# Optimization experiments

Hardware: AMD Instinct MI355X
Metric: run time of the kernel (lower is better)

## Reference

```python
import math
import jax, jax.numpy as jnp
import numpy as np

V, D, DEPTH, H, DH, FF = 32000, 1024, 4, 16, 64, 4096
B, N = 1, 2048


def setup_inputs() -> dict:
    key = jax.random.key(0)
    ks = jax.random.split(key, 8)
    s = 0.02
    return {
        "x": jax.random.randint(ks[0], (B, N), 0, V, dtype=jnp.int32),
        "token_emb": jax.random.normal(ks[1], (V, D), jnp.float32) * s,
        "attn_gamma": jnp.ones((DEPTH, D), jnp.float32),
        "w_qkv": jax.random.normal(ks[2], (DEPTH, D, 3 * H * DH), jnp.float32) * s,
        "w_attn_out": jax.random.normal(ks[3], (DEPTH, H * DH, D), jnp.float32) * s,
        "ff_gamma": jnp.ones((DEPTH, D), jnp.float32),
        "w_ff1": jax.random.normal(ks[4], (DEPTH, D, FF), jnp.float32) * s,
        "b_ff1": jnp.zeros((DEPTH, FF), jnp.float32),
        "w_ff2": jax.random.normal(ks[5], (DEPTH, FF, D), jnp.float32) * s,
        "b_ff2": jnp.zeros((DEPTH, D), jnp.float32),
        "final_gamma": jnp.ones((D,), jnp.float32),
        "w_logits": jax.random.normal(ks[6], (D, V), jnp.float32) * s,
    }


def rms_norm(x, gamma):
    # F.normalize(x, dim=-1) * sqrt(D) * gamma
    norm = jnp.sqrt(jnp.sum(x * x, axis=-1, keepdims=True))
    return x / jnp.maximum(norm, 1e-12) * (x.shape[-1] ** 0.5) * gamma


def rope_cos_sin(n, dh, dtype):
    # lucidrains rotary-embedding-torch default: interleaved pairs
    inv_freq = 1.0 / (10000.0 ** (jnp.arange(0, dh, 2, dtype=jnp.float32) / dh))
    freqs = jnp.arange(n, dtype=jnp.float32)[:, None] * inv_freq[None, :]  # [n, dh/2]
    freqs = jnp.repeat(freqs, 2, axis=-1)  # [n, dh]
    return jnp.cos(freqs).astype(dtype), jnp.sin(freqs).astype(dtype)


def rotate_half(x):
    x1 = x[..., 0::2]
    x2 = x[..., 1::2]
    return jnp.stack((-x2, x1), axis=-1).reshape(x.shape)


def apply_rope(t, cos, sin):
    # t: [b, h, n, dh]; cos/sin: [n, dh]
    return t * cos[None, None] + rotate_half(t) * sin[None, None]


def decoder_forward(x, token_emb, attn_gamma, w_qkv, w_attn_out, ff_gamma,
                    w_ff1, b_ff1, w_ff2, b_ff2, final_gamma, w_logits):
    b, n = x.shape
    h = token_emb[x]  # [b, n, D]
    cos, sin = rope_cos_sin(n, DH, h.dtype)
    causal = jnp.triu(jnp.ones((n, n), bool), k=1)
    scale = DH ** -0.5
    neg = -jnp.finfo(h.dtype).max
    for l in range(DEPTH):
        # attention block
        xn = rms_norm(h, attn_gamma[l])
        qkv = xn @ w_qkv[l]  # [b, n, 3*H*DH]
        qkv = qkv.reshape(b, n, 3, H, DH).transpose(2, 0, 3, 1, 4)  # [3, b, H, n, DH]
        q, k, v = qkv[0], qkv[1], qkv[2]
        q = apply_rope(q, cos, sin)
        k = apply_rope(k, cos, sin)
        sim = jnp.einsum('bhid,bhjd->bhij', q, k) * scale
        sim = jnp.where(causal, neg, sim)
        attn = jax.nn.softmax(sim, axis=-1)
        out = jnp.einsum('bhij,bhjd->bhid', attn, v)
        out = out.transpose(0, 2, 1, 3).reshape(b, n, H * DH) @ w_attn_out[l]
        h = h + out
        # feedforward block
        fn = rms_norm(h, ff_gamma[l])
        ff = jax.nn.gelu(fn @ w_ff1[l] + b_ff1[l], approximate=False) @ w_ff2[l] + b_ff2[l]
        h = h + ff
    return rms_norm(h, final_gamma) @ w_logits


def reference(x, token_emb, attn_gamma, w_qkv, w_attn_out, ff_gamma,
              w_ff1, b_ff1, w_ff2, b_ff2, final_gamma, w_logits):
    return decoder_forward(x, token_emb, attn_gamma, w_qkv, w_attn_out, ff_gamma,
                           w_ff1, b_ff1, w_ff2, b_ff2, final_gamma, w_logits)
```

## Files before the change

### kernel.cpp

```cpp
#include <hip/hip_runtime.h>
#include <math.h>


#define NSEQ 2048
#define DMODEL 1024
#define NH 16
#define DHEAD 64
#define FFD 4096
#define VOC 32000
#define NLAYER 4

typedef unsigned short u16;
typedef short bf16x8 __attribute__((ext_vector_type(8)));
typedef float f32x4 __attribute__((ext_vector_type(4)));

__device__ __forceinline__ u16 f2bf(float f) {
  unsigned int u = __builtin_bit_cast(unsigned int, f);
  u += 0x7fffu + ((u >> 16) & 1u);
  return (u16)(u >> 16);
}

__device__ __forceinline__ void gload16(const void* g, void* l) {
  __builtin_amdgcn_global_load_lds((__attribute__((address_space(1))) void*)g,
                                   (__attribute__((address_space(3))) void*)l,
                                   16, 0, 0);
}

__device__ __forceinline__ f32x4 mfma16x32(bf16x8 a, bf16x8 b, f32x4 c) {
  return __builtin_amdgcn_mfma_f32_16x16x32_bf16(a, b, c, 0, 0, 0);
}

template <int N>
__device__ __forceinline__ void waitvm() {
  if constexpr (N == 0) asm volatile("s_waitcnt vmcnt(0)" ::: "memory");
  else if constexpr (N == 2) asm volatile("s_waitcnt vmcnt(2)" ::: "memory");
  else if constexpr (N == 3) asm volatile("s_waitcnt vmcnt(3)" ::: "memory");
  else if constexpr (N == 4) asm volatile("s_waitcnt vmcnt(4)" ::: "memory");
  else if constexpr (N == 6) asm volatile("s_waitcnt vmcnt(6)" ::: "memory");
  else if constexpr (N == 8) asm volatile("s_waitcnt vmcnt(8)" ::: "memory");
}


__global__ __launch_bounds__(256) void k_embed(const int* __restrict__ x,
                                               const float* __restrict__ emb,
                                               float* __restrict__ h) {
  const int n = blockIdx.x, t = threadIdx.x;
  const int tok = x[n];
  reinterpret_cast<float4*>(h + (size_t)n * DMODEL)[t] =
      reinterpret_cast<const float4*>(emb + (size_t)tok * DMODEL)[t];
}

__global__ void k_rope(float* __restrict__ ct, float* __restrict__ st) {
  const int n = blockIdx.x, p = threadIdx.x;
  const double inv = exp(-(double)(2 * p) / 64.0 * log(10000.0));
  const double a = (double)n * inv;
  ct[n * 32 + p] = (float)cos(a);
  st[n * 32 + p] = (float)sin(a);
}

__global__ __launch_bounds__(256) void k_transpose(const float* __restrict__ in0,
                                                   u16* __restrict__ out0,
                                                   int K, int Nc,
                                                   size_t ls_in, size_t ls_out) {
  const float* in = in0 + blockIdx.z * ls_in;
  u16* out = out0 + blockIdx.z * ls_out;
  __shared__ float tile[64][65];
  const int kb = blockIdx.x * 64, nb = blockIdx.y * 64;
  const int tr = threadIdx.x >> 4;
  const int tc = threadIdx.x & 15;
#pragma unroll
  for (int r = 0; r < 64; r += 16) {
    const float4 v = *reinterpret_cast<const float4*>(
        &in[(size_t)(kb + r + tr) * Nc + nb + tc * 4]);
    tile[r + tr][tc * 4 + 0] = v.x;
    tile[r + tr][tc * 4 + 1] = v.y;
    tile[r + tr][tc * 4 + 2] = v.z;
    tile[r + tr][tc * 4 + 3] = v.w;
  }
  __syncthreads();
#pragma unroll
  for (int r = 0; r < 64; r += 16) {
    const int n = r + tr;
    ushort4 o;
    o.x = f2bf(tile[tc * 4 + 0][n]);
    o.y = f2bf(tile[tc * 4 + 1][n]);
    o.z = f2bf(tile[tc * 4 + 2][n]);
    o.w = f2bf(tile[tc * 4 + 3][n]);
    *reinterpret_cast<ushort4*>(&out[(size_t)(nb + n) * K + kb + tc * 4]) = o;
  }
}

__global__ __launch_bounds__(256) void k_rmsnorm(const float* __restrict__ h,
                                                 const float* __restrict__ gamma,
                                                 u16* __restrict__ out) {
  __shared__ float red[4];
  const int n = blockIdx.x, t = threadIdx.x;
  const float4 v = reinterpret_cast<const float4*>(h + (size_t)n * DMODEL)[t];
  float ss = v.x * v.x + v.y * v.y + v.z * v.z + v.w * v.w;
#pragma unroll
  for (int off = 32; off; off >>= 1) ss += __shfl_down(ss, off);
  if ((t & 63) == 0) red[t >> 6] = ss;
  __syncthreads();
  const float tot = red[0] + red[1] + red[2] + red[3];
  const float inv = 32.0f / fmaxf(sqrtf(tot), 1e-12f);
  const float4 g = reinterpret_cast<const float4*>(gamma)[t];
  ushort4 o;
  o.x = f2bf(v.x * inv * g.x);
  o.y = f2bf(v.y * inv * g.y);
  o.z = f2bf(v.z * inv * g.z);
  o.w = f2bf(v.w * inv * g.w);
  reinterpret_cast<ushort4*>(out + (size_t)n * DMODEL)[t] = o;
}

#define EPI_STORE 0
#define EPI_ADD 1
#define EPI_GELU 2
#define EPI_BIAS_ADD 3
#define EPI_QKV 4

__device__ __forceinline__ bf16x8 ldsfragT(const char* base, int row, int lg) {
  return *reinterpret_cast<const bf16x8*>(
      base + row * 64 + (((lg ^ (row & 3) ^ ((row >> 2) & 3)) & 3) << 4));
}

template <int EPI, int BM, int BN>
__global__ __launch_bounds__(256) void k_gemmT(
    const u16* __restrict__ A, const u16* __restrict__ BT, int K, int Nc,
    int NMB, const float* __restrict__ bias, const float* __restrict__ add,
    float* __restrict__ outf, u16* __restrict__ outb,
    u16* __restrict__ Qr, u16* __restrict__ Kr, u16* __restrict__ VT,
    const float* __restrict__ ct, const float* __restrict__ st) {
  constexpr int MFR = BM / 32;
  constexpr int NFR = BN / 32;
  constexpr int ABYTES = BM * 64;
  constexpr int BBYTES = BN * 64;
  constexpr int BUFB = ABYTES + BBYTES;
  constexpr int SL = BM / 64 + BN / 64;
  __shared__ alignas(16) char sm[4 * BUFB];
  const int nt = K >> 5;
  const int nwg = gridDim.x;
  int swz = blockIdx.x;
  if ((nwg & 7) == 0) swz = (swz & 7) * (nwg >> 3) + (swz >> 3);
  const int mb = swz % NMB, nb = swz / NMB;
  const int m0 = mb * BM, n0 = nb * BN;

  const int tid = threadIdx.x, w = tid >> 6, lane = tid & 63;
  const int wr = w >> 1, wc = w & 1;
  const int lr = lane & 15, lg = lane >> 4;

  const int srow = tid >> 2;
  const int gslot = (tid & 3) ^ (srow & 3) ^ ((srow >> 2) & 3);
  const u16* ga0 = A + (size_t)(m0 + srow) * K + gslot * 8;
  const u16* ga1 = A + (size_t)(m0 + (BM == 128 ? 64 : 0) + srow) * K + gslot * 8;
  const u16* gb0 = BT + (size_t)(n0 + srow) * K + gslot * 8;
  const u16* gb1 = BT + (size_t)(n0 + (BN == 128 ? 64 : 0) + srow) * K + gslot * 8;
  const int ldOff = tid * 16;

  auto stage = [&](int b) {
    char* base = sm + b * BUFB;
    gload16(ga0, base + ldOff);
    if constexpr (BM == 128) gload16(ga1, base + 4096 + ldOff);
    gload16(gb0, base + ABYTES + ldOff);
    if constexpr (BN == 128) gload16(gb1, base + ABYTES + 4096 + ldOff);
    ga0 += 32; gb0 += 32;
    if constexpr (BM == 128) ga1 += 32;
    if constexpr (BN == 128) gb1 += 32;
  };

  stage(0);
  stage(1);
  stage(2);
  waitvm<2 * SL>();
  __builtin_amdgcn_s_barrier();

  f32x4 acc[MFR][NFR] = {};
  int cur = 0;
  for (int t = 0; t < nt; ++t) {
    const char* Ab = sm + cur * BUFB;
    const char* Bb = Ab + ABYTES;
    bf16x8 af[MFR], bf[NFR];
#pragma unroll
    for (int i = 0; i < MFR; ++i)
      af[i] = ldsfragT(Ab, wr * (BM / 2) + i * 16 + lr, lg);
#pragma unroll
    for (int i = 0; i < NFR; ++i)
      bf[i] = ldsfragT(Bb, wc * (BN / 2) + i * 16 + lr, lg);
    if (t + 3 < nt) stage((cur + 3) & 3);
    __builtin_amdgcn_s_setprio(1);
#pragma unroll
    for (int mi = 0; mi < MFR; ++mi)
#pragma unroll
      for (int nj = 0; nj < NFR; ++nj)
        acc[mi][nj] = mfma16x32(af[mi], bf[nj], acc[mi][nj]);
    __builtin_amdgcn_s_setprio(0);
    if (t + 1 < nt) {
      __builtin_amdgcn_sched_barrier(0);
      if (t + 3 < nt)      waitvm<2 * SL>();
      else if (t + 2 < nt) waitvm<SL>();
      else                 waitvm<0>();
      __builtin_amdgcn_s_barrier();
      __builtin_amdgcn_sched_barrier(0);
    }
    cur = (cur + 1) & 3;
  }

  if constexpr (EPI == EPI_QKV) {
    const int which = n0 >> 10;
    const int hh = ((n0 & 1023) >> 6) + wc;
#pragma unroll
    for (int mi = 0; mi < MFR; ++mi) {
#pragma unroll
      for (int nj = 0; nj < NFR; ++nj) {
        const int d = nj * 16 + lr;
#pragma unroll
        for (int r = 0; r < 4; ++r) {
          const int row = m0 + wr * (BM / 2) + mi * 16 + lg * 4 + r;
          const float v = acc[mi][nj][r];
          if (which == 2) {
            VT[((size_t)hh * DHEAD + d) * NSEQ + row] = f2bf(v);
          } else {
            const float part = __shfl_xor(v, 1);
            const float sgn = (d & 1) ? 1.0f : -1.0f;
            const float c = ct[row * 32 + (d >> 1)];
            const float s_ = st[row * 32 + (d >> 1)];
            const u16 o = f2bf(v * c + sgn * part * s_);
            u16* dst = (which == 0) ? Qr : Kr;
            dst[((size_t)hh * NSEQ + row) * DHEAD + d] = o;
          }
        }
      }
    }
    return;
  }
#pragma unroll
  for (int mi = 0; mi < MFR; ++mi) {
#pragma unroll
    for (int nj = 0; nj < NFR; ++nj) {
      const int col = n0 + wc * (BN / 2) + nj * 16 + lr;
#pragma unroll
      for (int r = 0; r < 4; ++r) {
        const int row = m0 + wr * (BM / 2) + mi * 16 + lg * 4 + r;
        const size_t idx = (size_t)row * Nc + col;
        float v = acc[mi][nj][r];
        if (EPI == EPI_GELU) {
          v += bias[col];
          v = 0.5f * v * (1.0f + erff(v * 0.70710678118654752f));
          outb[idx] = f2bf(v);
        } else if (EPI == EPI_ADD) {
          outf[idx] = v + add[idx];
        } else if (EPI == EPI_BIAS_ADD) {
          outf[idx] = v + bias[col] + add[idx];
        } else {
          outf[idx] = v;
        }
      }
    }
  }
}

template <int EPI>
__global__ __launch_bounds__(256, 2) void k_gemmW(
    const u16* __restrict__ A, const u16* __restrict__ BT, int K, int Nc,
    const float* __restrict__ bias, float* __restrict__ outf,
    u16* __restrict__ outb) {
  constexpr int ABYTES = 8192;
  constexpr int BUFB = ABYTES + 16384;
  __shared__ alignas(16) char sm[3 * BUFB];
  const int nt = K >> 5;
  const int NMB = 16;
  const int nwg = gridDim.x;
  int swz = blockIdx.x;
  if ((nwg & 7) == 0) swz = (swz & 7) * (nwg >> 3) + (swz >> 3);
  const int mb = swz % NMB, nb = swz / NMB;
  const int m0 = mb * 128, n0 = nb * 256;

  const int tid = threadIdx.x, w = tid >> 6, lane = tid & 63;
  const int wr = w >> 1, wc = w & 1;
  const int lr = lane & 15, lg = lane >> 4;

  const int srow = tid >> 2;
  const int gslot = (tid & 3) ^ (srow & 3) ^ ((srow >> 2) & 3);
  const u16* ga0 = A + (size_t)(m0 + srow) * K + gslot * 8;
  const u16* ga1 = A + (size_t)(m0 + 64 + srow) * K + gslot * 8;
  const u16* gb0 = BT + (size_t)(n0 + srow) * K + gslot * 8;
  const u16* gb1 = BT + (size_t)(n0 + 64 + srow) * K + gslot * 8;
  const u16* gb2 = BT + (size_t)(n0 + 128 + srow) * K + gslot * 8;
  const u16* gb3 = BT + (size_t)(n0 + 192 + srow) * K + gslot * 8;
  const int ldOff = tid * 16;

  auto stage = [&](int b) {
    char* base = sm + b * BUFB;
    gload16(ga0, base + ldOff);
    gload16(ga1, base + 4096 + ldOff);
    gload16(gb0, base + ABYTES + ldOff);
    gload16(gb1, base + ABYTES + 4096 + ldOff);
    gload16(gb2, base + ABYTES + 8192 + ldOff);
    gload16(gb3, base + ABYTES + 12288 + ldOff);
    ga0 += 32; ga1 += 32; gb0 += 32; gb1 += 32; gb2 += 32; gb3 += 32;
  };

  stage(0);
  stage(1);
  waitvm<6>();
  __builtin_amdgcn_s_barrier();

  f32x4 acc[4][8] = {};
  int cur = 0, nx2 = 2;
  for (int t = 0; t < nt; ++t) {
    const char* Ab = sm + cur * BUFB;
    const char* Bb = Ab + ABYTES;
    const bool pf = (t + 2 < nt);
    bf16x8 af[4], bf[8];
#pragma unroll
    for (int i = 0; i < 4; ++i)
      af[i] = ldsfragT(Ab, wr * 64 + i * 16 + lr, lg);
#pragma unroll
    for (int i = 0; i < 8; ++i)
      bf[i] = ldsfragT(Bb, wc * 128 + i * 16 + lr, lg);
    if (pf) stage(nx2);
    __builtin_amdgcn_s_setprio(1);
#pragma unroll
    for (int mi = 0; mi < 4; ++mi)
#pragma unroll
      for (int nj = 0; nj < 8; ++nj)
        acc[mi][nj] = mfma16x32(af[mi], bf[nj], acc[mi][nj]);
    __builtin_amdgcn_s_setprio(0);
    if (t + 1 < nt) {
      __builtin_amdgcn_sched_barrier(0);
      if (pf) waitvm<6>();
      else    waitvm<0>();
      __builtin_amdgcn_s_barrier();
      __builtin_amdgcn_sched_barrier(0);
    }
    cur = (cur == 2) ? 0 : cur + 1;
    nx2 = (nx2 == 2) ? 0 : nx2 + 1;
  }

#pragma unroll
  for (int mi = 0; mi < 4; ++mi) {
#pragma unroll
    for (int nj = 0; nj < 8; ++nj) {
      const int col = n0 + wc * 128 + nj * 16 + lr;
#pragma unroll
      for (int r = 0; r < 4; ++r) {
        const int row = m0 + wr * 64 + mi * 16 + lg * 4 + r;
        const size_t idx = (size_t)row * Nc + col;
        float v = acc[mi][nj][r];
        if (EPI == EPI_GELU) {
          v += bias[col];
          v = 0.5f * v * (1.0f + erff(v * 0.70710678118654752f));
          outb[idx] = f2bf(v);
        } else {
          outf[idx] = v;
        }
      }
    }
  }
}

__global__ __launch_bounds__(256) void k_attn(const u16* __restrict__ Qr,
                                              const u16* __restrict__ Kr,
                                              const u16* __restrict__ VT,
                                              u16* __restrict__ O) {
  __shared__ alignas(16) u16 Pl[4][16 * 32];
  const int id = blockIdx.x;
  int qb, hh;
  if (id < 256) { qb = id & 31; hh = id >> 5; }
  else          { qb = 31 - (id & 31); hh = 8 + ((id - 256) >> 5); }
  const int w = threadIdx.x >> 6, lane = threadIdx.x & 63;
  const int lr = lane & 15, lg = lane >> 4;
  const int q0 = qb * 64 + w * 16;
  const u16* Qh = Qr + (size_t)hh * NSEQ * DHEAD;
  const u16* Kh = Kr + (size_t)hh * NSEQ * DHEAD;
  const u16* Vh = VT + (size_t)hh * DHEAD * NSEQ;
  u16* Pw = Pl[w];

  const bf16x8 aq0 = *reinterpret_cast<const bf16x8*>(Qh + (q0 + lr) * DHEAD + lg * 8);
  const bf16x8 aq1 = *reinterpret_cast<const bf16x8*>(Qh + (q0 + lr) * DHEAD + 32 + lg * 8);

  f32x4 o0 = {}, o1 = {}, o2 = {}, o3 = {};
  float m[4], l[4];
#pragma unroll
  for (int r = 0; r < 4; ++r) { m[r] = -1e30f; l[r] = 0.0f; }

  const int jend = q0 + 15;

  auto loadK = [&](int j0, bf16x8* bk) {
    bk[0] = *reinterpret_cast<const bf16x8*>(Kh + (j0 + lr) * DHEAD + lg * 8);
    bk[1] = *reinterpret_cast<const bf16x8*>(Kh + (j0 + lr) * DHEAD + 32 + lg * 8);
    bk[2] = *reinterpret_cast<const bf16x8*>(Kh + (j0 + 16 + lr) * DHEAD + lg * 8);
    bk[3] = *reinterpret_cast<const bf16x8*>(Kh + (j0 + 16 + lr) * DHEAD + 32 + lg * 8);
  };
  auto loadV = [&](int j0, bf16x8* vv) {
    const u16* vb = Vh + j0 + lg * 8;
    vv[0] = *reinterpret_cast<const bf16x8*>(vb + (0 + lr) * NSEQ);
    vv[1] = *reinterpret_cast<const bf16x8*>(vb + (16 + lr) * NSEQ);
    vv[2] = *reinterpret_cast<const bf16x8*>(vb + (32 + lr) * NSEQ);
    vv[3] = *reinterpret_cast<const bf16x8*>(vb + (48 + lr) * NSEQ);
  };

  bf16x8 bk[4], vv[4], bkN[4], vvN[4];
  loadK(0, bk);
  loadV(0, vv);

  for (int j0 = 0; j0 <= jend; j0 += 32) {
    if (j0 + 32 <= jend) { loadK(j0 + 32, bkN); loadV(j0 + 32, vvN); }

    f32x4 s0 = {}, s1 = {};
    s0 = mfma16x32(aq0, bk[0], s0);
    s0 = mfma16x32(aq1, bk[1], s0);
    s1 = mfma16x32(aq0, bk[2], s1);
    s1 = mfma16x32(aq1, bk[3], s1);

    float sv0[4], sv1[4], pm[4];
#pragma unroll
    for (int r = 0; r < 4; ++r) {
      const int irow = q0 + lg * 4 + r;
      sv0[r] = (j0 + lr > irow) ? -1e30f : s0[r] * 0.125f;
      sv1[r] = (j0 + 16 + lr > irow) ? -1e30f : s1[r] * 0.125f;
      pm[r] = fmaxf(sv0[r], sv1[r]);
    }
#pragma unroll
    for (int off = 1; off < 16; off <<= 1)
#pragma unroll
      for (int r = 0; r < 4; ++r) pm[r] = fmaxf(pm[r], __shfl_xor(pm[r], off));
    float p0[4], p1[4], rs[4];
    f32x4 fv;
#pragma unroll
    for (int r = 0; r < 4; ++r) {
      const float mn = fmaxf(m[r], pm[r]);
      fv[r] = __expf(m[r] - mn);
      m[r] = mn;
      p0[r] = __expf(sv0[r] - mn);
      p1[r] = __expf(sv1[r] - mn);
      rs[r] = p0[r] + p1[r];
    }
#pragma unroll
    for (int off = 1; off < 16; off <<= 1)
#pragma unroll
      for (int r = 0; r < 4; ++r) rs[r] += __shfl_xor(rs[r], off);
#pragma unroll
    for (int r = 0; r < 4; ++r) l[r] = l[r] * fv[r] + rs[r];
    o0 *= fv; o1 *= fv; o2 *= fv; o3 *= fv;

#pragma unroll
    for (int r = 0; r < 4; ++r) {
      Pw[(lg * 4 + r) * 32 + lr] = f2bf(p0[r]);
      Pw[(lg * 4 + r) * 32 + 16 + lr] = f2bf(p1[r]);
    }
    const bf16x8 pa = *reinterpret_cast<const bf16x8*>(Pw + lr * 32 + lg * 8);
    o0 = mfma16x32(pa, vv[0], o0);
    o1 = mfma16x32(pa, vv[1], o1);
    o2 = mfma16x32(pa, vv[2], o2);
    o3 = mfma16x32(pa, vv[3], o3);

#pragma unroll
    for (int i = 0; i < 4; ++i) { bk[i] = bkN[i]; vv[i] = vvN[i]; }
  }

#pragma unroll
  for (int r = 0; r < 4; ++r) {
    const int row = q0 + lg * 4 + r;
    const float invl = 1.0f / l[r];
    u16* orow = O + (size_t)row * DMODEL + hh * DHEAD;
    orow[0 * 16 + lr] = f2bf(o0[r] * invl);
    orow[1 * 16 + lr] = f2bf(o1[r] * invl);
    orow[2 * 16 + lr] = f2bf(o2[r] * invl);
    orow[3 * 16 + lr] = f2bf(o3[r] * invl);
  }
}


extern "C" void kernel_launch(void* const* d_in, const int* in_sizes, int n_in,
                              void* d_out, int out_size, void* d_ws, size_t ws_size,
                              hipStream_t stream) {
  (void)in_sizes; (void)n_in;
  const int* x = (const int*)d_in[0];
  const float* emb = (const float*)d_in[1];
  const float* attn_gamma = (const float*)d_in[2];
  const float* w_qkv = (const float*)d_in[3];
  const float* w_attn_out = (const float*)d_in[4];
  const float* ff_gamma = (const float*)d_in[5];
  const float* w_ff1 = (const float*)d_in[6];
  const float* b_ff1 = (const float*)d_in[7];
  const float* w_ff2 = (const float*)d_in[8];
  const float* b_ff2 = (const float*)d_in[9];
  const float* final_gamma = (const float*)d_in[10];
  const float* w_logits = (const float*)d_in[11];
  float* out = (float*)d_out;

  const size_t EARLY_NEED = 176ull << 20;
  const size_t FINAL_NEED = 72ull << 20;
  char* earlyBase;
  char* finalBase;
  if (ws_size >= EARLY_NEED + FINAL_NEED) {
    earlyBase = (char*)d_ws;
    finalBase = (char*)d_ws + EARLY_NEED;
  } else if (ws_size >= FINAL_NEED && (size_t)out_size * 4 >= EARLY_NEED) {
    earlyBase = (char*)d_out;
    finalBase = (char*)d_ws;
  } else {
    return;
  }
  size_t eoff = 0, foff = 0;
  auto ealloc = [&](size_t b) { void* p = earlyBase + eoff; eoff += (b + 255) & ~(size_t)255; return p; };
  auto falloc = [&](size_t b) { void* p = finalBase + foff; foff += (b + 255) & ~(size_t)255; return p; };

  u16* wqkvT = (u16*)ealloc((size_t)NLAYER * 3072 * DMODEL * 2);
  u16* wattnT = (u16*)ealloc((size_t)NLAYER * DMODEL * DMODEL * 2);
  u16* wff1T = (u16*)ealloc((size_t)NLAYER * FFD * DMODEL * 2);
  u16* wff2T = (u16*)ealloc((size_t)NLAYER * DMODEL * FFD * 2);
  float* h = (float*)ealloc((size_t)NSEQ * DMODEL * 4);
  u16* Qr = (u16*)ealloc((size_t)NH * NSEQ * DHEAD * 2);
  u16* Kr = (u16*)ealloc((size_t)NH * NSEQ * DHEAD * 2);
  u16* VTb = (u16*)ealloc((size_t)NH * NSEQ * DHEAD * 2);
  u16* Ob = (u16*)ealloc((size_t)NSEQ * DMODEL * 2);
  u16* ff1b = (u16*)ealloc((size_t)NSEQ * FFD * 2);
  float* ct = (float*)ealloc((size_t)NSEQ * 32 * 4);
  float* st = (float*)ealloc((size_t)NSEQ * 32 * 4);
  u16* wlogT = (u16*)falloc((size_t)VOC * DMODEL * 2);
  u16* xn = (u16*)falloc((size_t)NSEQ * DMODEL * 2);

  k_rope<<<dim3(NSEQ), dim3(32), 0, stream>>>(ct, st);
  k_transpose<<<dim3(16, 48, NLAYER), 256, 0, stream>>>(
      w_qkv, wqkvT, DMODEL, 3072, (size_t)DMODEL * 3072, (size_t)3072 * DMODEL);
  k_transpose<<<dim3(16, 16, NLAYER), 256, 0, stream>>>(
      w_attn_out, wattnT, DMODEL, DMODEL, (size_t)DMODEL * DMODEL, (size_t)DMODEL * DMODEL);
  k_transpose<<<dim3(16, 64, NLAYER), 256, 0, stream>>>(
      w_ff1, wff1T, DMODEL, FFD, (size_t)DMODEL * FFD, (size_t)FFD * DMODEL);
  k_transpose<<<dim3(64, 16, NLAYER), 256, 0, stream>>>(
      w_ff2, wff2T, FFD, DMODEL, (size_t)FFD * DMODEL, (size_t)DMODEL * FFD);
  k_transpose<<<dim3(16, 500, 1), 256, 0, stream>>>(
      w_logits, wlogT, DMODEL, VOC, 0, 0);

  k_embed<<<dim3(NSEQ), 256, 0, stream>>>(x, emb, h);

  for (int lyr = 0; lyr < NLAYER; ++lyr) {
    k_rmsnorm<<<dim3(NSEQ), 256, 0, stream>>>(h, attn_gamma + (size_t)lyr * DMODEL, xn);
    k_gemmT<EPI_QKV, 64, 128><<<dim3(32 * 24), 256, 0, stream>>>(
        xn, wqkvT + (size_t)lyr * 3072 * DMODEL, DMODEL, 3072, 32,
        nullptr, nullptr, nullptr, nullptr, Qr, Kr, VTb, ct, st);
    k_attn<<<dim3(512), 256, 0, stream>>>(Qr, Kr, VTb, Ob);
    k_gemmT<EPI_ADD, 64, 64><<<dim3(32 * 16), 256, 0, stream>>>(
        Ob, wattnT + (size_t)lyr * DMODEL * DMODEL, DMODEL, DMODEL, 32,
        nullptr, h, h, nullptr, nullptr, nullptr, nullptr, nullptr, nullptr);
    k_rmsnorm<<<dim3(NSEQ), 256, 0, stream>>>(h, ff_gamma + (size_t)lyr * DMODEL, xn);
    k_gemmT<EPI_GELU, 64, 128><<<dim3(32 * 32), 256, 0, stream>>>(
        xn, wff1T + (size_t)lyr * FFD * DMODEL, DMODEL, FFD, 32,
        b_ff1 + (size_t)lyr * FFD, nullptr, nullptr, ff1b,
        nullptr, nullptr, nullptr, nullptr, nullptr);
    k_gemmT<EPI_BIAS_ADD, 64, 64><<<dim3(32 * 16), 256, 0, stream>>>(
        ff1b, wff2T + (size_t)lyr * DMODEL * FFD, FFD, DMODEL, 32,
        b_ff2 + (size_t)lyr * DMODEL, h, h, nullptr,
        nullptr, nullptr, nullptr, nullptr, nullptr);
  }

  k_rmsnorm<<<dim3(NSEQ), 256, 0, stream>>>(h, final_gamma, xn);
  k_gemmW<EPI_STORE><<<dim3(16 * 125), 256, 0, stream>>>(
      xn, wlogT, DMODEL, VOC, nullptr, out, nullptr);
}
```

Before: 1.205 ms.

## Split-K the FF2 GEMM with atomic residual accumulation; nontemporal weight/logit stores

The FF2 GEMM (K=4096) is split into two K halves, launched as twice as many workgroups, and each half atomically adds its partial result plus bias (first half only) into the residual h, so the separate read of the add buffer goes away. The goal is better CU occupancy for a long-K GEMM that had only 512 tiles. Separately, the weight-transpose and logits output stores become nontemporal to reduce cache pollution. Atomics add contention and make the float summation order nondeterministic.

```diff
diff --git a/kernel.cpp b/kernel.cpp
--- a/kernel.cpp
+++ b/kernel.cpp
@@ -86,7 +86,10 @@
     o.y = f2bf(tile[tc * 4 + 1][n]);
     o.z = f2bf(tile[tc * 4 + 2][n]);
     o.w = f2bf(tile[tc * 4 + 3][n]);
-    *reinterpret_cast<ushort4*>(&out[(size_t)(nb + n) * K + kb + tc * 4]) = o;
+    const unsigned long long ull = __builtin_bit_cast(unsigned long long, o);
+    __builtin_nontemporal_store(
+        ull, reinterpret_cast<unsigned long long*>(
+                 &out[(size_t)(nb + n) * K + kb + tc * 4]));
   }
 }
 
@@ -117,13 +120,14 @@
 #define EPI_GELU 2
 #define EPI_BIAS_ADD 3
 #define EPI_QKV 4
+#define EPI_ATOM 5
 
 __device__ __forceinline__ bf16x8 ldsfragT(const char* base, int row, int lg) {
   return *reinterpret_cast<const bf16x8*>(
       base + row * 64 + (((lg ^ (row & 3) ^ ((row >> 2) & 3)) & 3) << 4));
 }
 
-template <int EPI, int BM, int BN>
+template <int EPI, int BM, int BN, int KSPLIT>
 __global__ __launch_bounds__(256) void k_gemmT(
     const u16* __restrict__ A, const u16* __restrict__ BT, int K, int Nc,
     int NMB, const float* __restrict__ bias, const float* __restrict__ add,
@@ -138,11 +142,20 @@
   constexpr int SL = BM / 64 + BN / 64;
   __shared__ alignas(16) char sm[4 * BUFB];
   const int nt = K >> 5;
-  const int nwg = gridDim.x;
-  int swz = blockIdx.x;
-  if ((nwg & 7) == 0) swz = (swz & 7) * (nwg >> 3) + (swz >> 3);
+  int bid = blockIdx.x;
+  int ksp = 0;
+  int inner = gridDim.x;
+  if constexpr (KSPLIT == 2) {
+    inner = gridDim.x >> 1;
+    ksp = bid / inner;
+    bid = bid % inner;
+  }
+  int swz = bid;
+  if ((inner & 7) == 0) swz = (swz & 7) * (inner >> 3) + (swz >> 3);
   const int mb = swz % NMB, nb = swz / NMB;
   const int m0 = mb * BM, n0 = nb * BN;
+  const int lda = K * KSPLIT;
+  const size_t kofs = (size_t)ksp * K;
 
   const int tid = threadIdx.x, w = tid >> 6, lane = tid & 63;
   const int wr = w >> 1, wc = w & 1;
@@ -150,10 +163,10 @@
 
   const int srow = tid >> 2;
   const int gslot = (tid & 3) ^ (srow & 3) ^ ((srow >> 2) & 3);
-  const u16* ga0 = A + (size_t)(m0 + srow) * K + gslot * 8;
-  const u16* ga1 = A + (size_t)(m0 + (BM == 128 ? 64 : 0) + srow) * K + gslot * 8;
-  const u16* gb0 = BT + (size_t)(n0 + srow) * K + gslot * 8;
-  const u16* gb1 = BT + (size_t)(n0 + (BN == 128 ? 64 : 0) + srow) * K + gslot * 8;
+  const u16* ga0 = A + (size_t)(m0 + srow) * lda + kofs + gslot * 8;
+  const u16* ga1 = A + (size_t)(m0 + (BM == 128 ? 64 : 0) + srow) * lda + kofs + gslot * 8;
+  const u16* gb0 = BT + (size_t)(n0 + srow) * lda + kofs + gslot * 8;
+  const u16* gb1 = BT + (size_t)(n0 + (BN == 128 ? 64 : 0) + srow) * lda + kofs + gslot * 8;
   const int ldOff = tid * 16;
 
   auto stage = [&](int b) {
@@ -242,7 +255,10 @@
         const int row = m0 + wr * (BM / 2) + mi * 16 + lg * 4 + r;
         const size_t idx = (size_t)row * Nc + col;
         float v = acc[mi][nj][r];
-        if (EPI == EPI_GELU) {
+        if (EPI == EPI_ATOM) {
+          if (ksp == 0) v += bias[col];
+          atomicAdd(&outf[idx], v);
+        } else if (EPI == EPI_GELU) {
           v += bias[col];
           v = 0.5f * v * (1.0f + erff(v * 0.70710678118654752f));
           outb[idx] = f2bf(v);
@@ -351,7 +367,7 @@
           v = 0.5f * v * (1.0f + erff(v * 0.70710678118654752f));
           outb[idx] = f2bf(v);
         } else {
-          outf[idx] = v;
+          __builtin_nontemporal_store(v, &outf[idx]);
         }
       }
     }
@@ -537,21 +553,21 @@
 
   for (int lyr = 0; lyr < NLAYER; ++lyr) {
     k_rmsnorm<<<dim3(NSEQ), 256, 0, stream>>>(h, attn_gamma + (size_t)lyr * DMODEL, xn);
-    k_gemmT<EPI_QKV, 64, 128><<<dim3(32 * 24), 256, 0, stream>>>(
+    k_gemmT<EPI_QKV, 64, 128, 1><<<dim3(32 * 24), 256, 0, stream>>>(
         xn, wqkvT + (size_t)lyr * 3072 * DMODEL, DMODEL, 3072, 32,
         nullptr, nullptr, nullptr, nullptr, Qr, Kr, VTb, ct, st);
     k_attn<<<dim3(512), 256, 0, stream>>>(Qr, Kr, VTb, Ob);
-    k_gemmT<EPI_ADD, 64, 64><<<dim3(32 * 16), 256, 0, stream>>>(
+    k_gemmT<EPI_ADD, 64, 64, 1><<<dim3(32 * 16), 256, 0, stream>>>(
         Ob, wattnT + (size_t)lyr * DMODEL * DMODEL, DMODEL, DMODEL, 32,
         nullptr, h, h, nullptr, nullptr, nullptr, nullptr, nullptr, nullptr);
     k_rmsnorm<<<dim3(NSEQ), 256, 0, stream>>>(h, ff_gamma + (size_t)lyr * DMODEL, xn);
-    k_gemmT<EPI_GELU, 64, 128><<<dim3(32 * 32), 256, 0, stream>>>(
+    k_gemmT<EPI_GELU, 64, 128, 1><<<dim3(32 * 32), 256, 0, stream>>>(
         xn, wff1T + (size_t)lyr * FFD * DMODEL, DMODEL, FFD, 32,
         b_ff1 + (size_t)lyr * FFD, nullptr, nullptr, ff1b,
         nullptr, nullptr, nullptr, nullptr, nullptr);
-    k_gemmT<EPI_BIAS_ADD, 64, 64><<<dim3(32 * 16), 256, 0, stream>>>(
-        ff1b, wff2T + (size_t)lyr * DMODEL * FFD, FFD, DMODEL, 32,
-        b_ff2 + (size_t)lyr * DMODEL, h, h, nullptr,
+    k_gemmT<EPI_ATOM, 64, 64, 2><<<dim3(32 * 16 * 2), 256, 0, stream>>>(
+        ff1b, wff2T + (size_t)lyr * DMODEL * FFD, FFD / 2, DMODEL, 32,
+        b_ff2 + (size_t)lyr * DMODEL, nullptr, h, nullptr,
         nullptr, nullptr, nullptr, nullptr, nullptr);
   }
 
```

New measurement: 1.194 ms. About the same (-0.9%).
